# Kernel tuning notes

Measured on AMD Instinct MI355X. Metric: run time of the kernel, lower is better.

Reference implementation:

```python
import jax, jax.numpy as jnp
import numpy as np

EPS = 1e-5  # BatchNorm eps (inference mode: running_mean=0, running_var=1)


def _bn(x, gamma, beta):
    # eval-mode BatchNorm1d over channel dim of (B, C, N)
    scale = gamma / jnp.sqrt(1.0 + EPS)
    return x * scale[None, :, None] + beta[None, :, None]


def setup_inputs() -> dict:
    key = jax.random.key(0)
    ks = jax.random.split(key, 9)
    B, C, N = 16, 512, 4096
    h, k, u, m = 4, 16, 4, 7
    v = 512 // h  # dim_v = out_channels // nhead = 128
    x = jax.random.normal(ks[0], (B, C, N), jnp.float32)
    Wq = jax.random.normal(ks[1], (k * h, C), jnp.float32) * 0.05
    gq = 1.0 + 0.1 * jax.random.normal(ks[2], (k * h,), jnp.float32)
    bq = 0.1 * jax.random.normal(ks[3], (k * h,), jnp.float32)
    Wk = jax.random.normal(ks[4], (k * u, C), jnp.float32) * 0.05
    Wv = jax.random.normal(ks[5], (v * u, C), jnp.float32) * 0.05
    gv = 1.0 + 0.1 * jax.random.normal(ks[6], (v * u,), jnp.float32)
    bv = 0.1 * jax.random.normal(ks[7], (v * u,), jnp.float32)
    emb = jax.random.normal(ks[8], (k, u, 1, m), jnp.float32)  # Conv2d weight (O,I,1,m)
    return {"x": x, "Wq": Wq, "gq": gq, "bq": bq, "Wk": Wk,
            "Wv": Wv, "gv": gv, "bv": bv, "emb": emb}


def reference(x, Wq, gq, bq, Wk, Wv, gv, bv, emb):
    B, C, N = x.shape
    k, u, _, m = emb.shape
    h = Wq.shape[0] // k
    v = Wv.shape[0] // u
    pad = (m - 1) // 2
    # 1x1 conv projections == channel matmuls
    queries = _bn(jnp.einsum('oc,bcn->bon', Wq, x), gq, bq).reshape(B, h, k, N)
    keys = jax.nn.softmax(
        jnp.einsum('oc,bcn->bon', Wk, x).reshape(B, k, u, N), axis=-1)
    values = _bn(jnp.einsum('oc,bcn->bon', Wv, x), gv, bv).reshape(B, v, u, N)
    # content lambda: (B, k, v)
    lambda_c = jnp.einsum('bkun,bvun->bkv', keys, values)
    y_c = jnp.einsum('bhkn,bkv->bhvn', queries, lambda_c)
    # position lambda via conv2d over reinterpreted values (B, u, v, N)
    values_2d = values.reshape(B, u, v, N)
    lambda_p = jax.lax.conv_general_dilated(
        values_2d, emb, window_strides=(1, 1),
        padding=[(0, 0), (pad, pad)],
        dimension_numbers=('NCHW', 'OIHW', 'NCHW'))  # (B, k, v, N)
    y_p = jnp.einsum('bhkn,bkvn->bhvn', queries, lambda_p)
    return (y_c + y_p).reshape(B, h * v, N)
```

## Files before the change

### kernel.cpp

```cpp
#include <hip/hip_runtime.h>
#include <hip/hip_bf16.h>


#define B_  16
#define C_  512
#define N_  4096
#define OT  640

typedef __bf16 bf16x8 __attribute__((ext_vector_type(8)));
typedef float  f32x4  __attribute__((ext_vector_type(4)));

static constexpr size_t PBF_OFF = 0;
static constexpr size_t XT_OFF  = ((size_t)B_ * OT * N_) / 2;
static constexpr size_t WB_OFF  = XT_OFF + ((size_t)B_ * N_ * C_) / 2;
static constexpr size_t SB_OFF  = WB_OFF + ((size_t)OT * C_) / 2;
static constexpr size_t ST_OFF  = SB_OFF + (size_t)OT * 2;
static constexpr size_t LAM_OFF = ST_OFF + (size_t)B_ * 64 * 2;

__device__ __forceinline__ void load_lds16(const void* g, void* l) {
  __builtin_amdgcn_global_load_lds(
      (const __attribute__((address_space(1))) void*)g,
      (__attribute__((address_space(3))) void*)l, 16, 0, 0);
}

__device__ __forceinline__ unsigned short f2bf(float f) {
  __hip_bfloat16 h = __float2bfloat16(f);
  return *(unsigned short*)&h;
}
__device__ __forceinline__ float bf2f(unsigned short u) {
  union { unsigned int i; float f; } c; c.i = ((unsigned int)u) << 16; return c.f;
}

__global__ __launch_bounds__(256) void pack_kernel(
    const float* __restrict__ Wq, const float* __restrict__ gq, const float* __restrict__ bq,
    const float* __restrict__ Wk, const float* __restrict__ Wv,
    const float* __restrict__ gv, const float* __restrict__ bv,
    __hip_bfloat16* __restrict__ Wall, float* __restrict__ sb) {
  int idx = blockIdx.x * 256 + threadIdx.x;
  if (idx < OT * C_) {
    int row = idx >> 9;
    float val;
    if (row < 64)        val = Wq[idx];
    else if (row < 128)  val = Wk[idx - 64 * C_];
    else                 val = Wv[idx - 128 * C_];
    Wall[idx] = __float2bfloat16(val);
  }
  if (idx < OT) {
    const float inv = 0.99999500003749971875f;
    float s, bi;
    if (idx < 64)       { s = gq[idx] * inv;       bi = bq[idx]; }
    else if (idx < 128) { s = 1.0f;                bi = 0.0f; }
    else                { s = gv[idx - 128] * inv; bi = bv[idx - 128]; }
    sb[idx * 2]     = s;
    sb[idx * 2 + 1] = bi;
  }
}

__global__ __launch_bounds__(256) void convert_x(
    const float* __restrict__ x, __hip_bfloat16* __restrict__ xT) {
  const int n0 = blockIdx.x * 64;
  const int c0 = blockIdx.y * 64;
  const int b  = blockIdx.z;
  __shared__ float tile[64][65];
  const int t = threadIdx.x;
  const int tr = t >> 4, tc4 = (t & 15) * 4;
  const float* xb = x + ((size_t)b * C_ + c0) * N_ + n0;
#pragma unroll
  for (int i = 0; i < 4; ++i) {
    float4 v = *(const float4*)&xb[(size_t)(i * 16 + tr) * N_ + tc4];
    *(float4*)&tile[i * 16 + tr][tc4] = v;
  }
  __syncthreads();
  __hip_bfloat16* ob = xT + ((size_t)b * N_ + n0) * C_ + c0;
#pragma unroll
  for (int i = 0; i < 4; ++i) {
    int rn = i * 16 + tr;
    uint2 pk;
    __hip_bfloat16* ph = (__hip_bfloat16*)&pk;
#pragma unroll
    for (int j = 0; j < 4; ++j) ph[j] = __float2bfloat16(tile[tc4 + j][rn]);
    *(uint2*)&ob[(size_t)rn * C_ + tc4] = pk;
  }
}

__global__ __launch_bounds__(256) void gemm_mfma(
    const __hip_bfloat16* __restrict__ xT, const __hip_bfloat16* __restrict__ Wb,
    const float* __restrict__ sb, __hip_bfloat16* __restrict__ pbf) {
  const int t = threadIdx.x;
  const int l = t & 63, w = t >> 6;
  const int wr = w >> 1, wc = w & 1;
  const int m0 = blockIdx.y * 128, n0 = blockIdx.x * 128;
  const int b = blockIdx.z;
  const __hip_bfloat16* xb = xT + (size_t)b * N_ * C_;

  __shared__ __hip_bfloat16 Als[128 * 32];
  __shared__ __hip_bfloat16 Bls[128 * 32];

  const int srow = w * 16 + (l >> 2);
  const int scol = (l & 3) * 8;
  const __hip_bfloat16* gA = Wb + (size_t)(m0 + srow) * C_ + scol;
  const __hip_bfloat16* gB = xb + (size_t)(n0 + srow) * C_ + scol;
  __hip_bfloat16* lA = &Als[w * 512 + l * 8];
  __hip_bfloat16* lB = &Bls[w * 512 + l * 8];

  const int fr = l & 15;
  const int kg = (l >> 4) * 8;

  f32x4 acc[4][4] = {};

  for (int c0 = 0; c0 < C_; c0 += 32) {
    __syncthreads();
#pragma unroll
    for (int i = 0; i < 2; ++i) {
      load_lds16(gA + (size_t)i * 64 * C_ + c0, lA + i * 2048);
      load_lds16(gB + (size_t)i * 64 * C_ + c0, lB + i * 2048);
    }
    __syncthreads();
    bf16x8 af[4], bfr[4];
#pragma unroll
    for (int m = 0; m < 4; ++m)
      af[m] = *(const bf16x8*)&Als[(size_t)(wr * 64 + m * 16 + fr) * 32 + kg];
#pragma unroll
    for (int n = 0; n < 4; ++n)
      bfr[n] = *(const bf16x8*)&Bls[(size_t)(wc * 64 + n * 16 + fr) * 32 + kg];
#pragma unroll
    for (int m = 0; m < 4; ++m)
#pragma unroll
      for (int n = 0; n < 4; ++n)
        acc[m][n] = __builtin_amdgcn_mfma_f32_16x16x32_bf16(af[m], bfr[n], acc[m][n], 0, 0, 0);
  }

  __hip_bfloat16* pb = pbf + (size_t)b * OT * N_;
  const int rb = (l >> 4) * 4;
#pragma unroll
  for (int m = 0; m < 4; ++m) {
#pragma unroll
    for (int r = 0; r < 4; ++r) {
      int grow = m0 + wr * 64 + m * 16 + rb + r;
      float s = sb[grow * 2], bi = sb[grow * 2 + 1];
#pragma unroll
      for (int n = 0; n < 4; ++n) {
        int gcol = n0 + wc * 64 + n * 16 + fr;
        pb[(size_t)grow * N_ + gcol] = __float2bfloat16(acc[m][n][r] * s + bi);
      }
    }
  }
}

__global__ __launch_bounds__(256) void softmax_stats(
    const __hip_bfloat16* __restrict__ pbf, float* __restrict__ stats) {
  const int r = blockIdx.x, b = blockIdx.y;
  const __hip_bfloat16* row = pbf + ((size_t)b * OT + 64 + r) * N_;
  const int t = threadIdx.x;
  float f[16];
  {
    uint4 v1 = ((const uint4*)row)[t];
    uint4 v2 = ((const uint4*)row)[t + 256];
    const unsigned short* h1 = (const unsigned short*)&v1;
    const unsigned short* h2 = (const unsigned short*)&v2;
#pragma unroll
    for (int j = 0; j < 8; ++j) { f[j] = bf2f(h1[j]); f[j + 8] = bf2f(h2[j]); }
  }
  float mx = -1e30f;
#pragma unroll
  for (int j = 0; j < 16; ++j) mx = fmaxf(mx, f[j]);
  __shared__ float red[4];
#pragma unroll
  for (int off = 32; off; off >>= 1) mx = fmaxf(mx, __shfl_xor(mx, off));
  if ((t & 63) == 0) red[t >> 6] = mx;
  __syncthreads();
  mx = fmaxf(fmaxf(red[0], red[1]), fmaxf(red[2], red[3]));
  float sum = 0.f;
#pragma unroll
  for (int j = 0; j < 16; ++j) sum += __expf(f[j] - mx);
  __syncthreads();
#pragma unroll
  for (int off = 32; off; off >>= 1) sum += __shfl_xor(sum, off);
  if ((t & 63) == 0) red[t >> 6] = sum;
  __syncthreads();
  if (t == 0) {
    float s = red[0] + red[1] + red[2] + red[3];
    stats[((size_t)b * 64 + r) * 2]     = mx;
    stats[((size_t)b * 64 + r) * 2 + 1] = 1.0f / s;
  }
}

__global__ __launch_bounds__(256) void lambda_c_kernel(
    const __hip_bfloat16* __restrict__ pbf, const float* __restrict__ stats,
    float* __restrict__ lam) {
  const int ns = blockIdx.x;
  const int b  = blockIdx.y;
  const int nb = ns * 128;
  const int t = threadIdx.x, l = t & 63, w = t >> 6;
  __shared__ __hip_bfloat16 klds[64 * 128];

  const __hip_bfloat16* kg = pbf + ((size_t)b * OT + 64) * N_ + nb;
  const float* stb = stats + (size_t)b * 64 * 2;
#pragma unroll
  for (int i = 0; i < 4; ++i) {
    int task = i * 256 + t;
    int row = task >> 4, gc = task & 15;
    uint4 val = *(const uint4*)&kg[(size_t)row * N_ + gc * 8];
    float mx = stb[row * 2], ivs = stb[row * 2 + 1];
    unsigned short* hs = (unsigned short*)&val;
#pragma unroll
    for (int j = 0; j < 8; ++j)
      hs[j] = f2bf(__expf(bf2f(hs[j]) - mx) * ivs);
    int byte = (row * 256 + gc * 16) ^ (((row >> 2) & 7) << 4);
    *(uint4*)((char*)klds + byte) = val;
  }
  __syncthreads();

  const int fr = l & 15, g = l >> 4;
  const __hip_bfloat16* vg = pbf + ((size_t)b * OT + 128) * N_ + nb;
  float* lamb = lam + (size_t)b * 16 * 128;
#pragma unroll
  for (int vt = 0; vt < 2; ++vt) {
    const int vv0 = (vt * 4 + w) * 16;
    f32x4 acc = {};
#pragma unroll
    for (int ui = 0; ui < 4; ++ui) {
#pragma unroll
      for (int s = 0; s < 4; ++s) {
        const int krow = fr * 4 + ui;
        const int byte = (krow * 256 + s * 64 + g * 16) ^ (((krow >> 2) & 7) << 4);
        bf16x8 af = *(const bf16x8*)((const char*)klds + byte);
        const int vrow = (vv0 + fr) * 4 + ui;
        bf16x8 bf = *(const bf16x8*)&vg[(size_t)vrow * N_ + s * 32 + g * 8];
        acc = __builtin_amdgcn_mfma_f32_16x16x32_bf16(af, bf, acc, 0, 0, 0);
      }
    }
#pragma unroll
    for (int r = 0; r < 4; ++r)
      atomicAdd(&lamb[(g * 4 + r) * 128 + vv0 + fr], acc[r]);
  }
}

__global__ __launch_bounds__(256) void final_kernel(
    const __hip_bfloat16* __restrict__ pbf, const float* __restrict__ lam,
    const float* __restrict__ emb, float* __restrict__ out) {
  const int n0  = blockIdx.x * 32;
  const int vq  = blockIdx.y;
  const int b   = blockIdx.z;
  const int vv0 = vq * 32;
  const __hip_bfloat16* qb = pbf + (size_t)b * OT * N_;
  const __hip_bfloat16* vb = pbf + ((size_t)b * OT + 128) * N_;
  const int t = threadIdx.x, l = t & 63, w = t >> 6;

  __shared__ __hip_bfloat16 P_lds[32][40][4];
  __shared__ float lamT[32][16];

  const int fr = l & 15;
  const int g  = l >> 4;
  const int rb = g * 4;
  const int gb0 = g & 1, gb1 = g >> 1;

  union { uint4 u; bf16x8 v; } ef;
  {
    unsigned short eh[8];
#pragma unroll
    for (int j = 0; j < 8; ++j) {
      int kap = g * 8 + j;
      float val = 0.f;
      if (kap < 28) val = emb[fr * 28 + (kap & 3) * 7 + (kap >> 2)];
      eh[j] = f2bf(val);
    }
    ef.u.x = eh[0] | ((unsigned)eh[1] << 16);
    ef.u.y = eh[2] | ((unsigned)eh[3] << 16);
    ef.u.z = eh[4] | ((unsigned)eh[5] << 16);
    ef.u.w = eh[6] | ((unsigned)eh[7] << 16);
  }

  float qreg[4][4][2];
#pragma unroll
  for (int hh = 0; hh < 4; ++hh)
#pragma unroll
    for (int r = 0; r < 4; ++r)
#pragma unroll
      for (int nt = 0; nt < 2; ++nt)
        qreg[hh][r][nt] = bf2f(*(const unsigned short*)
            &qb[(size_t)(hh * 16 + rb + r) * N_ + n0 + nt * 16 + fr]);

#pragma unroll
  for (int i = 0; i < 5; ++i) {
    int task = i * 256 + t;
    int vl = task / 40;
    int np = task - vl * 40;
    int gn = n0 + np - 3;
    unsigned short hv[4];
    if (np < 38 && gn >= 0 && gn < N_) {
#pragma unroll
      for (int ui = 0; ui < 4; ++ui)
        hv[ui] = *(const unsigned short*)&vb[(size_t)(ui * 128 + vv0 + vl) * N_ + gn];
    } else {
      hv[0] = hv[1] = hv[2] = hv[3] = 0;
    }
    uint2 pk;
    pk.x = hv[0] | ((unsigned)hv[1] << 16);
    pk.y = hv[2] | ((unsigned)hv[3] << 16);
    *(uint2*)&P_lds[vl][np][0] = pk;
  }
  {
    int kk = t >> 5, vl = t & 31;
    lamT[vl][kk]     = lam[((size_t)b * 16 + kk) * 128 + vv0 + vl];
    lamT[vl][kk + 8] = lam[((size_t)b * 16 + kk + 8) * 128 + vv0 + vl];
  }
  __syncthreads();

  float* obase = out + ((size_t)b * 512 + g * 128 + vv0) * N_ + n0;
#pragma unroll
  for (int mi = 0; mi < 16; ++mi) {
    const int vl_t = w * 8 + (mi >> 1);
    const int nt   = mi & 1;
    const int nlc  = nt * 16 + fr;
    union { uint4 u; bf16x8 v; } bf;
    {
      const uint2 lo = *(const uint2*)&P_lds[vl_t][nlc + 2 * g][0];
      const uint2 hi = *(const uint2*)&P_lds[vl_t][nlc + 2 * g + 1][0];
      bf.u.x = lo.x; bf.u.y = lo.y; bf.u.z = hi.x; bf.u.w = hi.y;
    }
    f32x4 c = *(const f32x4*)&lamT[vl_t][rb];
    f32x4 d = __builtin_amdgcn_mfma_f32_16x16x32_bf16(ef.v, bf.v, c, 0, 0, 0);
    float p0 = qreg[0][0][nt] * d[0] + qreg[0][1][nt] * d[1] + qreg[0][2][nt] * d[2] + qreg[0][3][nt] * d[3];
    float p1 = qreg[1][0][nt] * d[0] + qreg[1][1][nt] * d[1] + qreg[1][2][nt] * d[2] + qreg[1][3][nt] * d[3];
    float p2 = qreg[2][0][nt] * d[0] + qreg[2][1][nt] * d[1] + qreg[2][2][nt] * d[2] + qreg[2][3][nt] * d[3];
    float p3 = qreg[3][0][nt] * d[0] + qreg[3][1][nt] * d[1] + qreg[3][2][nt] * d[2] + qreg[3][3][nt] * d[3];
    float e0 = gb0 ? p0 : p1;
    float e1 = gb0 ? p2 : p3;
    float s0 = (gb0 ? p1 : p0) + __shfl_xor(e0, 16);
    float s1 = (gb0 ? p3 : p2) + __shfl_xor(e1, 16);
    float e2 = gb1 ? s0 : s1;
    float yv = (gb1 ? s1 : s0) + __shfl_xor(e2, 32);
    obase[(size_t)vl_t * N_ + nlc] = yv;
  }
}

extern "C" void kernel_launch(void* const* d_in, const int* in_sizes, int n_in,
                              void* d_out, int out_size, void* d_ws, size_t ws_size,
                              hipStream_t stream) {
  const float* x   = (const float*)d_in[0];
  const float* Wq  = (const float*)d_in[1];
  const float* gq  = (const float*)d_in[2];
  const float* bq  = (const float*)d_in[3];
  const float* Wk  = (const float*)d_in[4];
  const float* Wv  = (const float*)d_in[5];
  const float* gv  = (const float*)d_in[6];
  const float* bv  = (const float*)d_in[7];
  const float* emb = (const float*)d_in[8];

  float* ws = (float*)d_ws;
  __hip_bfloat16* pbf   = (__hip_bfloat16*)(ws + PBF_OFF);
  __hip_bfloat16* xTb   = (__hip_bfloat16*)(ws + XT_OFF);
  __hip_bfloat16* Wallb = (__hip_bfloat16*)(ws + WB_OFF);
  float* sb    = ws + SB_OFF;
  float* stats = ws + ST_OFF;
  float* lam   = ws + LAM_OFF;
  float* out   = (float*)d_out;

  hipMemsetAsync(lam, 0, (size_t)B_ * 16 * 128 * sizeof(float), stream);
  pack_kernel<<<dim3(1280), 256, 0, stream>>>(Wq, gq, bq, Wk, Wv, gv, bv, Wallb, sb);
  convert_x<<<dim3(N_ / 64, C_ / 64, B_), 256, 0, stream>>>(x, xTb);
  gemm_mfma<<<dim3(N_ / 128, OT / 128, B_), 256, 0, stream>>>(xTb, Wallb, sb, pbf);
  softmax_stats<<<dim3(64, B_), 256, 0, stream>>>(pbf, stats);
  lambda_c_kernel<<<dim3(32, 16), 256, 0, stream>>>(pbf, stats, lam);
  final_kernel<<<dim3(N_ / 32, 4, B_), 256, 0, stream>>>(pbf, lam, emb, out);
}
```

Baseline: 202.2 us.

## Widen final kernel N tile and replace shuffle reduction with rotated MFMA passes

The final kernel now covers 64 positions per block instead of 32, so the staged value halo and lambda tile are amortized over more output columns. Each lane now holds four rotated copies of the embedding fragment and runs four MFMAs per output, accumulating over heads in registers, which removes the cross-lane shuffle reduction. The cost is four times the MFMA work per output, more registers, and per-tile query loads issued from global memory.

```diff
diff --git a/kernel.cpp b/kernel.cpp
--- a/kernel.cpp
+++ b/kernel.cpp
@@ -239,7 +239,7 @@
 __global__ __launch_bounds__(256) void final_kernel(
     const __hip_bfloat16* __restrict__ pbf, const float* __restrict__ lam,
     const float* __restrict__ emb, float* __restrict__ out) {
-  const int n0  = blockIdx.x * 32;
+  const int n0  = blockIdx.x * 64;
   const int vq  = blockIdx.y;
   const int b   = blockIdx.z;
   const int vv0 = vq * 32;
@@ -247,48 +247,38 @@
   const __hip_bfloat16* vb = pbf + ((size_t)b * OT + 128) * N_;
   const int t = threadIdx.x, l = t & 63, w = t >> 6;
 
-  __shared__ __hip_bfloat16 P_lds[32][40][4];
+  __shared__ __hip_bfloat16 P_lds[32][72][4];
   __shared__ float lamT[32][16];
 
   const int fr = l & 15;
   const int g  = l >> 4;
-  const int rb = g * 4;
-  const int gb0 = g & 1, gb1 = g >> 1;
-
-  union { uint4 u; bf16x8 v; } ef;
-  {
+
+  union { uint4 u; bf16x8 v; } ef[4];
+#pragma unroll
+  for (int j = 0; j < 4; ++j) {
+    const int krow = (fr + 4 * j) & 15;
     unsigned short eh[8];
 #pragma unroll
-    for (int j = 0; j < 8; ++j) {
-      int kap = g * 8 + j;
+    for (int j8 = 0; j8 < 8; ++j8) {
+      int kap = g * 8 + j8;
       float val = 0.f;
-      if (kap < 28) val = emb[fr * 28 + (kap & 3) * 7 + (kap >> 2)];
-      eh[j] = f2bf(val);
-    }
-    ef.u.x = eh[0] | ((unsigned)eh[1] << 16);
-    ef.u.y = eh[2] | ((unsigned)eh[3] << 16);
-    ef.u.z = eh[4] | ((unsigned)eh[5] << 16);
-    ef.u.w = eh[6] | ((unsigned)eh[7] << 16);
-  }
-
-  float qreg[4][4][2];
-#pragma unroll
-  for (int hh = 0; hh < 4; ++hh)
-#pragma unroll
-    for (int r = 0; r < 4; ++r)
-#pragma unroll
-      for (int nt = 0; nt < 2; ++nt)
-        qreg[hh][r][nt] = bf2f(*(const unsigned short*)
-            &qb[(size_t)(hh * 16 + rb + r) * N_ + n0 + nt * 16 + fr]);
-
-#pragma unroll
-  for (int i = 0; i < 5; ++i) {
+      if (kap < 28) val = emb[krow * 28 + (kap & 3) * 7 + (kap >> 2)];
+      eh[j8] = f2bf(val);
+    }
+    ef[j].u.x = eh[0] | ((unsigned)eh[1] << 16);
+    ef[j].u.y = eh[2] | ((unsigned)eh[3] << 16);
+    ef[j].u.z = eh[4] | ((unsigned)eh[5] << 16);
+    ef[j].u.w = eh[6] | ((unsigned)eh[7] << 16);
+  }
+
+#pragma unroll
+  for (int i = 0; i < 9; ++i) {
     int task = i * 256 + t;
-    int vl = task / 40;
-    int np = task - vl * 40;
+    int vl = task / 72;
+    int np = task - vl * 72;
     int gn = n0 + np - 3;
     unsigned short hv[4];
-    if (np < 38 && gn >= 0 && gn < N_) {
+    if (np < 70 && gn >= 0 && gn < N_) {
 #pragma unroll
       for (int ui = 0; ui < 4; ++ui)
         hv[ui] = *(const unsigned short*)&vb[(size_t)(ui * 128 + vv0 + vl) * N_ + gn];
@@ -309,29 +299,32 @@
 
   float* obase = out + ((size_t)b * 512 + g * 128 + vv0) * N_ + n0;
 #pragma unroll
-  for (int mi = 0; mi < 16; ++mi) {
-    const int vl_t = w * 8 + (mi >> 1);
-    const int nt   = mi & 1;
-    const int nlc  = nt * 16 + fr;
-    union { uint4 u; bf16x8 v; } bf;
-    {
-      const uint2 lo = *(const uint2*)&P_lds[vl_t][nlc + 2 * g][0];
-      const uint2 hi = *(const uint2*)&P_lds[vl_t][nlc + 2 * g + 1][0];
-      bf.u.x = lo.x; bf.u.y = lo.y; bf.u.z = hi.x; bf.u.w = hi.y;
-    }
-    f32x4 c = *(const f32x4*)&lamT[vl_t][rb];
-    f32x4 d = __builtin_amdgcn_mfma_f32_16x16x32_bf16(ef.v, bf.v, c, 0, 0, 0);
-    float p0 = qreg[0][0][nt] * d[0] + qreg[0][1][nt] * d[1] + qreg[0][2][nt] * d[2] + qreg[0][3][nt] * d[3];
-    float p1 = qreg[1][0][nt] * d[0] + qreg[1][1][nt] * d[1] + qreg[1][2][nt] * d[2] + qreg[1][3][nt] * d[3];
-    float p2 = qreg[2][0][nt] * d[0] + qreg[2][1][nt] * d[1] + qreg[2][2][nt] * d[2] + qreg[2][3][nt] * d[3];
-    float p3 = qreg[3][0][nt] * d[0] + qreg[3][1][nt] * d[1] + qreg[3][2][nt] * d[2] + qreg[3][3][nt] * d[3];
-    float e0 = gb0 ? p0 : p1;
-    float e1 = gb0 ? p2 : p3;
-    float s0 = (gb0 ? p1 : p0) + __shfl_xor(e0, 16);
-    float s1 = (gb0 ? p3 : p2) + __shfl_xor(e1, 16);
-    float e2 = gb1 ? s0 : s1;
-    float yv = (gb1 ? s1 : s0) + __shfl_xor(e2, 32);
-    obase[(size_t)vl_t * N_ + nlc] = yv;
+  for (int nt = 0; nt < 4; ++nt) {
+    const int nlc = nt * 16 + fr;
+    float qreg[16];
+#pragma unroll
+    for (int kk = 0; kk < 16; ++kk)
+      qreg[kk] = bf2f(*(const unsigned short*)&qb[(size_t)(g * 16 + kk) * N_ + n0 + nlc]);
+#pragma unroll
+    for (int vt = 0; vt < 8; ++vt) {
+      const int vl_t = w * 8 + vt;
+      union { uint4 u; bf16x8 v; } bfr;
+      {
+        const uint2 lo = *(const uint2*)&P_lds[vl_t][nlc + 2 * g][0];
+        const uint2 hi = *(const uint2*)&P_lds[vl_t][nlc + 2 * g + 1][0];
+        bfr.u.x = lo.x; bfr.u.y = lo.y; bfr.u.z = hi.x; bfr.u.w = hi.y;
+      }
+      float y = 0.f;
+#pragma unroll
+      for (int j = 0; j < 4; ++j) {
+        const int kb = 4 * ((g + j) & 3);
+        f32x4 c = *(const f32x4*)&lamT[vl_t][kb];
+        f32x4 d = __builtin_amdgcn_mfma_f32_16x16x32_bf16(ef[j].v, bfr.v, c, 0, 0, 0);
+        y += qreg[kb + 0] * d[0] + qreg[kb + 1] * d[1]
+           + qreg[kb + 2] * d[2] + qreg[kb + 3] * d[3];
+      }
+      obase[(size_t)vl_t * N_ + nlc] = y;
+    }
   }
 }
 
@@ -363,5 +356,5 @@
   gemm_mfma<<<dim3(N_ / 128, OT / 128, B_), 256, 0, stream>>>(xTb, Wallb, sb, pbf);
   softmax_stats<<<dim3(64, B_), 256, 0, stream>>>(pbf, stats);
   lambda_c_kernel<<<dim3(32, 16), 256, 0, stream>>>(pbf, stats, lam);
-  final_kernel<<<dim3(N_ / 32, 4, B_), 256, 0, stream>>>(pbf, lam, emb, out);
-}
+  final_kernel<<<dim3(N_ / 64, 4, B_), 256, 0, stream>>>(pbf, lam, emb, out);
+}
```

New measurement: 290.3 us. +43.6%, slower.

## Double-buffer LDS tiles in projection GEMM to overlap loads with MFMA

Applied to the files above, without the earlier changes.

The projection GEMM now keeps two LDS buffers for the A and B tiles and issues the global-to-LDS loads for the next K tile before running the MFMAs on the current one. This replaces two __syncthreads per iteration with a single explicit vmcnt wait and barrier, so memory latency can hide behind compute. In exchange it doubles the LDS footprint of the kernel, which could lower occupancy, and it depends on hand-placed waitcnt and barrier ordering being correct.

```diff
diff --git a/kernel.cpp b/kernel.cpp
--- a/kernel.cpp
+++ b/kernel.cpp
@@ -93,41 +93,57 @@
   const int b = blockIdx.z;
   const __hip_bfloat16* xb = xT + (size_t)b * N_ * C_;
 
-  __shared__ __hip_bfloat16 Als[128 * 32];
-  __shared__ __hip_bfloat16 Bls[128 * 32];
+  __shared__ __hip_bfloat16 Als[2][128 * 32];
+  __shared__ __hip_bfloat16 Bls[2][128 * 32];
 
   const int srow = w * 16 + (l >> 2);
   const int scol = (l & 3) * 8;
   const __hip_bfloat16* gA = Wb + (size_t)(m0 + srow) * C_ + scol;
   const __hip_bfloat16* gB = xb + (size_t)(n0 + srow) * C_ + scol;
-  __hip_bfloat16* lA = &Als[w * 512 + l * 8];
-  __hip_bfloat16* lB = &Bls[w * 512 + l * 8];
+  const int ldso = w * 512 + l * 8;
 
   const int fr = l & 15;
   const int kg = (l >> 4) * 8;
 
   f32x4 acc[4][4] = {};
 
-  for (int c0 = 0; c0 < C_; c0 += 32) {
-    __syncthreads();
-#pragma unroll
-    for (int i = 0; i < 2; ++i) {
-      load_lds16(gA + (size_t)i * 64 * C_ + c0, lA + i * 2048);
-      load_lds16(gB + (size_t)i * 64 * C_ + c0, lB + i * 2048);
-    }
-    __syncthreads();
+#pragma unroll
+  for (int i = 0; i < 2; ++i) {
+    load_lds16(gA + (size_t)i * 64 * C_, &Als[0][ldso + i * 2048]);
+    load_lds16(gB + (size_t)i * 64 * C_, &Bls[0][ldso + i * 2048]);
+  }
+  asm volatile("s_waitcnt vmcnt(0)" ::: "memory");
+  __builtin_amdgcn_s_barrier();
+  __builtin_amdgcn_sched_barrier(0);
+
+  int cur = 0;
+  for (int kt = 0; kt < 16; ++kt) {
+    if (kt < 15) {
+      const int c0n = (kt + 1) * 32;
+#pragma unroll
+      for (int i = 0; i < 2; ++i) {
+        load_lds16(gA + (size_t)i * 64 * C_ + c0n, &Als[cur ^ 1][ldso + i * 2048]);
+        load_lds16(gB + (size_t)i * 64 * C_ + c0n, &Bls[cur ^ 1][ldso + i * 2048]);
+      }
+    }
     bf16x8 af[4], bfr[4];
 #pragma unroll
     for (int m = 0; m < 4; ++m)
-      af[m] = *(const bf16x8*)&Als[(size_t)(wr * 64 + m * 16 + fr) * 32 + kg];
+      af[m] = *(const bf16x8*)&Als[cur][(size_t)(wr * 64 + m * 16 + fr) * 32 + kg];
 #pragma unroll
     for (int n = 0; n < 4; ++n)
-      bfr[n] = *(const bf16x8*)&Bls[(size_t)(wc * 64 + n * 16 + fr) * 32 + kg];
+      bfr[n] = *(const bf16x8*)&Bls[cur][(size_t)(wc * 64 + n * 16 + fr) * 32 + kg];
 #pragma unroll
     for (int m = 0; m < 4; ++m)
 #pragma unroll
       for (int n = 0; n < 4; ++n)
         acc[m][n] = __builtin_amdgcn_mfma_f32_16x16x32_bf16(af[m], bfr[n], acc[m][n], 0, 0, 0);
+    if (kt < 15) {
+      asm volatile("s_waitcnt vmcnt(0)" ::: "memory");
+      __builtin_amdgcn_s_barrier();
+      __builtin_amdgcn_sched_barrier(0);
+    }
+    cur ^= 1;
   }
 
   __hip_bfloat16* pb = pbf + (size_t)b * OT * N_;
```

Measured after the change: 205.9 us. No clear change (+1.8%).
